# Kernel optimization log

Hardware: AMD Instinct MI355X
Metric: run time of the kernel (lower is better)

## Reference

```python
import jax, jax.numpy as jnp
import numpy as np

B, S, HID = 2, 2048, 2304
H, KVH, D = 8, 4, 256          # query heads, kv heads, head_dim
N_REP = H // KVH
SCALE = 256.0 ** -0.5          # query_pre_attn_scalar ** -0.5
SOFTCAP = 50.0
ROPE_THETA = 10000.0
NEG = -1e9


def setup_inputs() -> dict:
    key = jax.random.key(0)
    k1, k2, k3, k4, k5 = jax.random.split(key, 5)
    hidden_states = jax.random.normal(k1, (B, S, HID), dtype=jnp.float32)
    # RoPE cos/sin tables, shape [B, S, D]
    inv_freq = 1.0 / (ROPE_THETA ** (jnp.arange(0, D, 2, dtype=jnp.float32) / D))
    pos = jnp.arange(S, dtype=jnp.float32)
    freqs = pos[:, None] * inv_freq[None, :]            # [S, D/2]
    emb = jnp.concatenate([freqs, freqs], axis=-1)      # [S, D]
    cos = jnp.broadcast_to(jnp.cos(emb)[None], (B, S, D))
    sin = jnp.broadcast_to(jnp.sin(emb)[None], (B, S, D))
    # additive causal mask [B, 1, S, S] (sliding_window=4096 > S, so pure causal)
    idx = jnp.arange(S)
    causal = idx[None, :] <= idx[:, None]
    attention_mask = jnp.broadcast_to(
        jnp.where(causal, 0.0, NEG).astype(jnp.float32)[None, None], (B, 1, S, S))
    # projection weights (lecun-normal-ish scale), no bias (attention_bias=False)
    Wq = jax.random.normal(k2, (HID, H * D), dtype=jnp.float32) / np.sqrt(HID)
    Wk = jax.random.normal(k3, (HID, KVH * D), dtype=jnp.float32) / np.sqrt(HID)
    Wv = jax.random.normal(k4, (HID, KVH * D), dtype=jnp.float32) / np.sqrt(HID)
    Wo = jax.random.normal(k5, (H * D, HID), dtype=jnp.float32) / np.sqrt(H * D)
    return {"hidden_states": hidden_states, "cos": cos, "sin": sin,
            "attention_mask": attention_mask,
            "Wq": Wq, "Wk": Wk, "Wv": Wv, "Wo": Wo}


def _rotate_half(x):
    half = x.shape[-1] // 2
    return jnp.concatenate([-x[..., half:], x[..., :half]], axis=-1)


def reference(hidden_states, cos, sin, attention_mask, Wq, Wk, Wv, Wo):
    b, s, _ = hidden_states.shape
    q = (hidden_states @ Wq).reshape(b, s, H, D).transpose(0, 2, 1, 3)    # [B,H,S,D]
    k = (hidden_states @ Wk).reshape(b, s, KVH, D).transpose(0, 2, 1, 3)  # [B,KVH,S,D]
    v = (hidden_states @ Wv).reshape(b, s, KVH, D).transpose(0, 2, 1, 3)
    c = cos[:, None]  # [B,1,S,D] broadcast over heads (unsqueeze_dim=1)
    sn = sin[:, None]
    q = q * c + _rotate_half(q) * sn
    k = k * c + _rotate_half(k) * sn
    # GQA: repeat kv heads (interleave, matching repeat_kv tile+reshape)
    k = jnp.repeat(k, N_REP, axis=1)
    v = jnp.repeat(v, N_REP, axis=1)
    w = jnp.einsum('bhqd,bhkd->bhqk', q, k) * SCALE
    w = jnp.tanh(w / SOFTCAP) * SOFTCAP                  # logit softcapping
    w = w + attention_mask[:, :, :, :s]
    w = jax.nn.softmax(w.astype(jnp.float32), axis=-1).astype(q.dtype)
    out = jnp.einsum('bhqk,bhkd->bhqd', w, v)
    out = out.transpose(0, 2, 1, 3).reshape(b, s, H * D)
    return out @ Wo
```

## Files before the change

### kernel.cpp

```cpp
#include <hip/hip_runtime.h>

typedef unsigned short u16;
typedef __attribute__((ext_vector_type(8))) short short8;
typedef __attribute__((ext_vector_type(4))) float f32x4;

constexpr int B_ = 2;
constexpr int H_ = 8;
constexpr int KVH_ = 4;
constexpr int S_ = 2048;
constexpr int D_ = 256;
constexpr int HID_ = 2304;
constexpr int QKVN_ = 4096;
constexpr int AON_ = 2048;

__device__ __forceinline__ float b2f(u16 u) {
  union { float f; unsigned int i; } x; x.i = ((unsigned int)u) << 16; return x.f;
}
__device__ __forceinline__ u16 f2b(float f) {
  unsigned int x = __float_as_uint(f);
  unsigned int r = (x + 0x7fffu + ((x >> 16) & 1u)) >> 16;
  return (u16)r;
}

__global__ void cast_kernel(const float* __restrict__ in, u16* __restrict__ out) {
  size_t i = ((size_t)blockIdx.x * 256 + threadIdx.x) * 4;
  float4 v = *(const float4*)(in + i);
  unsigned int lo = (unsigned int)f2b(v.x) | ((unsigned int)f2b(v.y) << 16);
  unsigned int hi = (unsigned int)f2b(v.z) | ((unsigned int)f2b(v.w) << 16);
  uint2 o; o.x = lo; o.y = hi;
  *(uint2*)(out + i) = o;
}

__global__ void transpose_cast_all(const float* __restrict__ s0, const float* __restrict__ s1,
                                   const float* __restrict__ s2, const float* __restrict__ s3,
                                   u16* __restrict__ d0, u16* __restrict__ d1,
                                   u16* __restrict__ d2, u16* __restrict__ d3) {
  __shared__ float tile[64][65];
  int which = blockIdx.z;
  const float* src; u16* dst; int R, C;
  if (which == 0)      { src = s0; dst = d0; R = 2304; C = 2048; }
  else if (which == 1) { src = s1; dst = d1; R = 2304; C = 1024; }
  else if (which == 2) { src = s2; dst = d2; R = 2304; C = 1024; }
  else                 { src = s3; dst = d3; R = 2048; C = 2304; }
  int r0 = blockIdx.y * 64, c0 = blockIdx.x * 64;
  if (r0 >= R || c0 >= C) return;
  int t = threadIdx.x;
#pragma unroll
  for (int i = 0; i < 16; ++i) {
    int e = i * 256 + t;
    int r = e >> 6, c = e & 63;
    tile[r][c] = src[(size_t)(r0 + r) * C + (c0 + c)];
  }
  __syncthreads();
#pragma unroll
  for (int i = 0; i < 16; ++i) {
    int e = i * 256 + t;
    int orow = e >> 6, ocol = e & 63;
    dst[(size_t)(c0 + orow) * R + (r0 + ocol)] = f2b(tile[ocol][orow]);
  }
}

template <int OUTF32>
__global__ __launch_bounds__(512, 2) void gemm_bt8(
    const u16* __restrict__ A, const u16* __restrict__ B, void* __restrict__ Cp,
    int M, int N, int K) {
  __shared__ u16 lds[2][2][2][8192];
  const int tid = threadIdx.x;
  const int lane = tid & 63;
  const int wave = tid >> 6;
  const int wm = wave >> 2, wn = wave & 3;
  const int quad = lane >> 4, l16 = lane & 15;
  const int m0 = blockIdx.y * 256, n0 = blockIdx.x * 256;
  const int nt = K >> 6;

  const int sub = tid >> 6;
  const int rr = (tid >> 2) & 15;
  const int cc = ((tid & 3) * 8) ^ ((rr & 8) ? 16 : 0);
  const int r_rel = (sub >> 1) * 16 + rr;
  const int ccol = (sub & 1) * 32 + cc;
  const u16* Asrc = A + (size_t)(m0 + r_rel) * K + ccol;
  const u16* Bsrc = B + (size_t)(n0 + r_rel) * K + ccol;
  const int ldsc = tid * 8;

  const int fr_off = l16 * 64 + (((quad * 8) ^ ((l16 & 8) ? 16 : 0)) << 1);

#define GL8(src, dst)                                                                  \
  __builtin_amdgcn_global_load_lds((const __attribute__((address_space(1))) void*)(src), \
                                   (__attribute__((address_space(3))) void*)(dst), 16, 0, 0)
#define STAGE_A(bf, kt, qp) {                                                          \
    const u16* _s = Asrc + (size_t)(kt) * 64;                                          \
    GL8(_s + (size_t)((qp) * 64) * K,       &lds[bf][0][0][(qp) * 4096 + ldsc]);       \
    GL8(_s + (size_t)(128 + (qp) * 64) * K, &lds[bf][0][1][(qp) * 4096 + ldsc]); }
#define STAGE_B(bf, kt, hf) {                                                          \
    const u16* _s = Bsrc + (size_t)(kt) * 64;                                          \
    GL8(_s + (size_t)((hf) * 128) * K,      &lds[bf][1][hf][ldsc]);                    \
    GL8(_s + (size_t)((hf) * 128 + 64) * K, &lds[bf][1][hf][4096 + ldsc]); }
#define LDA(bf, mi, kk) \
  (*(const short8*)((const char*)&lds[bf][0][wm][0] + (mi) * 2048 + (kk) * 1024 + fr_off))
#define LDB(bf, ni, kk) \
  (*(const short8*)((const char*)&lds[bf][1][wn >> 1][0] + ((wn & 1) * 4 + (ni)) * 2048 + (kk) * 1024 + fr_off))

  f32x4 acc[8][4] = {};
  short8 bfr[4][2], af[2][2];

  STAGE_B(0, 0, 0); STAGE_B(0, 0, 1); STAGE_A(0, 0, 0); STAGE_A(0, 0, 1);
  STAGE_B(1, 1, 0); STAGE_B(1, 1, 1); STAGE_A(1, 1, 0);
  asm volatile("s_waitcnt vmcnt(6)" ::: "memory");
  __builtin_amdgcn_s_barrier();

#define PHASE(q, STG, VMW)                                                             \
    _Pragma("unroll") for (int i = 0; i < 2; ++i)                                      \
      _Pragma("unroll") for (int kk = 0; kk < 2; ++kk) af[i][kk] = LDA(c, 2 * (q) + i, kk); \
    STG; VMW;                                                                          \
    __builtin_amdgcn_s_barrier();                                                      \
    asm volatile("s_waitcnt lgkmcnt(0)" ::: "memory");                                 \
    __builtin_amdgcn_sched_barrier(0);                                                 \
    __builtin_amdgcn_s_setprio(1);                                                     \
    _Pragma("unroll") for (int i = 0; i < 2; ++i)                                      \
      _Pragma("unroll") for (int ni = 0; ni < 4; ++ni)                                 \
        _Pragma("unroll") for (int kk = 0; kk < 2; ++kk)                               \
          acc[2 * (q) + i][ni] = __builtin_amdgcn_mfma_f32_16x16x32_bf16(              \
              af[i][kk], bfr[ni][kk], acc[2 * (q) + i][ni], 0, 0, 0);                  \
    __builtin_amdgcn_s_setprio(0);                                                     \
    __builtin_amdgcn_s_barrier();

  for (int T = 0; T < nt; ++T) {
    const int c = T & 1;
#pragma unroll
    for (int ni = 0; ni < 4; ++ni)
#pragma unroll
      for (int kk = 0; kk < 2; ++kk) bfr[ni][kk] = LDB(c, ni, kk);
    PHASE(0, if (T + 1 < nt) STAGE_A(c ^ 1, T + 1, 1), )
    PHASE(1, if (T + 2 < nt) STAGE_B(c, T + 2, 0), )
    PHASE(2, if (T + 2 < nt) STAGE_B(c, T + 2, 1), )
    PHASE(3, if (T + 2 < nt) STAGE_A(c, T + 2, 0),
          if (T + 2 >= nt) { asm volatile("s_waitcnt vmcnt(0)" ::: "memory"); }
          else             { asm volatile("s_waitcnt vmcnt(6)" ::: "memory"); })
  }
#undef PHASE
#undef LDA
#undef LDB
#undef STAGE_A
#undef STAGE_B
#undef GL8

#pragma unroll
  for (int mi = 0; mi < 8; ++mi) {
#pragma unroll
    for (int ni = 0; ni < 4; ++ni) {
#pragma unroll
      for (int r = 0; r < 4; ++r) {
        int row = m0 + wm * 128 + mi * 16 + quad * 4 + r;
        int col = n0 + wn * 64 + ni * 16 + l16;
        if (OUTF32)
          ((float*)Cp)[(size_t)row * N + col] = acc[mi][ni][r];
        else
          ((u16*)Cp)[(size_t)row * N + col] = f2b(acc[mi][ni][r]);
      }
    }
  }
}

__global__ void rope_kernel(const u16* __restrict__ qkv, const float* __restrict__ cs,
                            const float* __restrict__ sn, u16* __restrict__ Qr,
                            u16* __restrict__ Kr) {
  int row = blockIdx.x;
  int b = row >> 11, s = row & 2047;
  int d = threadIdx.x;
  const u16* qrow = qkv + (size_t)row * QKVN_;
  float c = cs[(size_t)row * D_ + d];
  float si = sn[(size_t)row * D_ + d];
  int dp = (d < 128) ? d + 128 : d - 128;
  float sgn = (d < 128) ? -1.f : 1.f;
#pragma unroll
  for (int h = 0; h < H_; ++h) {
    float v = b2f(qrow[h * D_ + d]);
    float p = sgn * b2f(qrow[h * D_ + dp]);
    Qr[((size_t)(b * H_ + h) * S_ + s) * D_ + d] = f2b(v * c + p * si);
  }
#pragma unroll
  for (int g = 0; g < KVH_; ++g) {
    float v = b2f(qrow[2048 + g * D_ + d]);
    float p = sgn * b2f(qrow[2048 + g * D_ + dp]);
    Kr[((size_t)(b * KVH_ + g) * S_ + s) * D_ + d] = f2b(v * c + p * si);
  }
}

__global__ void transpose_v(const u16* __restrict__ qkv, u16* __restrict__ Vt) {
  __shared__ u16 tile[64][72];
  int d0 = blockIdx.x * 64, s0 = blockIdx.y * 64, g = blockIdx.z;
  int b = g >> 2, kvh = g & 3;
  int t = threadIdx.x;
#pragma unroll
  for (int i = 0; i < 16; ++i) {
    int e = i * 256 + t;
    int r = e >> 6, c = e & 63;
    tile[r][c] = qkv[(size_t)(b * S_ + s0 + r) * QKVN_ + 3072 + kvh * D_ + d0 + c];
  }
  __syncthreads();
#pragma unroll
  for (int i = 0; i < 16; ++i) {
    int e = i * 256 + t;
    int orow = e >> 6, ocol = e & 63;
    Vt[((size_t)g * D_ + d0 + orow) * S_ + s0 + ocol] = tile[ocol][orow];
  }
}

__global__ __launch_bounds__(256, 2) void attn_kernel(
    const u16* __restrict__ Qr, const u16* __restrict__ Kr, const u16* __restrict__ Vt,
    float* __restrict__ Op0, float* __restrict__ Op1,
    float* __restrict__ Lp0, float* __restrict__ Lp1) {
  __shared__ u16 Ks[2][32 * 256];
  __shared__ u16 Vs[2][32 * 256];
  int bx = blockIdx.x;
  int b = bx >> 8;
  int r = bx & 255;
  int h = r >> 5;
  int rem = r & 31;
  int sp = rem >> 4;
  int t = rem & 15;
  int qt0 = (t & 1) ? (15 - (t >> 1)) : (t >> 1);
  int qt = b ? (15 - qt0) : qt0;
  int kvh = h >> 1;
  int tid = threadIdx.x, wave = tid >> 6, lane = tid & 63;
  int quad = lane >> 4, l16 = lane & 15;
  float* Op = sp ? Op1 : Op0;
  float* Lp = sp ? Lp1 : Lp0;
  const int kst_r = tid >> 5;
  const int kst_c = (tid & 31) ^ ((tid >> 5) & 3);
  const int vst_r = tid >> 2;
  const int vst_c = (tid & 3) ^ ((tid >> 3) & 3);
  const int kg = l16 >> 2, ka = l16 & 3;
  const int srow0 = 8 * kg + ka;
  const int ksw = ka | ((kg & 1) << 2);

  int q0 = qt * 128;
  int beg = sp ? (2 * qt + 2) : 0;
  int end = sp ? (4 * qt + 4) : (2 * qt + 2);
  const u16* Qbase = Qr + ((size_t)(b * H_ + h) * S_ + q0 + wave * 32 + l16) * D_;
  short8 qf[2][8];
#pragma unroll
  for (int f = 0; f < 2; ++f)
#pragma unroll
    for (int kk = 0; kk < 8; ++kk)
      qf[f][kk] = *(const short8*)(Qbase + (size_t)f * 16 * D_ + kk * 32 + quad * 8);
  const u16* Kbase = Kr + (size_t)(b * KVH_ + kvh) * S_ * D_;
  const u16* Vbase = Vt + (size_t)(b * KVH_ + kvh) * D_ * S_;
  float lp[2] = {0.f, 0.f};
  f32x4 o_acc[2][16] = {};
  const int qq0 = q0 + wave * 32 + l16;

#define STAGE(KT, BUF)                                                                 \
  {                                                                                    \
    int k0s = (KT) * 32;                                                               \
    _Pragma("unroll") for (int i = 0; i < 4; ++i) {                                    \
      int p = i * 256 + tid;                                                           \
      __builtin_amdgcn_global_load_lds(                                                \
          (const __attribute__((address_space(1))) void*)(Kbase +                      \
              (size_t)(k0s + i * 8 + kst_r) * D_ + (kst_c ^ ((i & 1) << 2)) * 8),      \
          (__attribute__((address_space(3))) void*)(&Ks[BUF][0] + p * 8), 16, 0, 0);   \
    }                                                                                  \
    _Pragma("unroll") for (int i = 0; i < 4; ++i) {                                    \
      int p = i * 256 + tid;                                                           \
      __builtin_amdgcn_global_load_lds(                                                \
          (const __attribute__((address_space(1))) void*)(Vbase +                      \
              (size_t)(i * 64 + vst_r) * S_ + k0s + vst_c * 8),                        \
          (__attribute__((address_space(3))) void*)(&Vs[BUF][0] + p * 8), 16, 0, 0);   \
    }                                                                                  \
  }

  STAGE(beg, 0);
  __syncthreads();
  for (int kt = beg; kt < end; ++kt) {
    int k0 = kt * 32;
    int cur = (kt - beg) & 1;
    if (kt + 1 < end) STAGE(kt + 1, cur ^ 1);
    f32x4 sacc[2][2] = {};
    __builtin_amdgcn_s_setprio(1);
#pragma unroll
    for (int n = 0; n < 2; ++n) {
      const u16* kb = &Ks[cur][0] + (srow0 + 4 * n) * 256;
#pragma unroll
      for (int kk = 0; kk < 8; ++kk) {
        int phys = (kk * 4 + quad) ^ ksw;
        short8 kfr = *(const short8*)(kb + phys * 8);
        sacc[0][n] = __builtin_amdgcn_mfma_f32_16x16x32_bf16(kfr, qf[0][kk], sacc[0][n], 0, 0, 0);
        sacc[1][n] = __builtin_amdgcn_mfma_f32_16x16x32_bf16(kfr, qf[1][kk], sacc[1][n], 0, 0, 0);
      }
    }
    __builtin_amdgcn_s_setprio(0);
    bool full = (k0 + 31 <= q0 + wave * 32);
    short8 pa[2];
#pragma unroll
    for (int f = 0; f < 2; ++f) {
      union { short8 s8; unsigned int d[4]; } pu;
#pragma unroll
      for (int n = 0; n < 2; ++n) {
#pragma unroll
        for (int rr2 = 0; rr2 < 4; ++rr2) {
          float E = __expf(sacc[f][n][rr2] * 0.0025f);
          float ee = __expf(-100.0f * __frcp_rn(E + 1.0f));
          if (!full) {
            int key = k0 + 8 * quad + 4 * n + rr2;
            ee = (key <= qq0 + f * 16) ? ee : 0.0f;
          }
          lp[f] += ee;
          sacc[f][n][rr2] = ee;
        }
        pu.d[2 * n]     = (unsigned int)f2b(sacc[f][n][0]) | ((unsigned int)f2b(sacc[f][n][1]) << 16);
        pu.d[2 * n + 1] = (unsigned int)f2b(sacc[f][n][2]) | ((unsigned int)f2b(sacc[f][n][3]) << 16);
      }
      pa[f] = pu.s8;
    }
    __builtin_amdgcn_s_setprio(1);
#pragma unroll
    for (int dt = 0; dt < 16; ++dt) {
      int d = dt * 16 + l16;
      int phys = quad ^ ((d >> 1) & 3);
      short8 vb = *(const short8*)(&Vs[cur][0] + d * 32 + phys * 8);
      o_acc[0][dt] = __builtin_amdgcn_mfma_f32_16x16x32_bf16(pa[0], vb, o_acc[0][dt], 0, 0, 0);
      o_acc[1][dt] = __builtin_amdgcn_mfma_f32_16x16x32_bf16(pa[1], vb, o_acc[1][dt], 0, 0, 0);
    }
    __builtin_amdgcn_s_setprio(0);
    __syncthreads();
  }
#undef STAGE
#pragma unroll
  for (int f = 0; f < 2; ++f) {
    lp[f] += __shfl_xor(lp[f], 16, 64);
    lp[f] += __shfl_xor(lp[f], 32, 64);
  }
  if (lane < 16) {
    size_t lb = ((size_t)(b * H_ + h)) * S_ + q0 + wave * 32 + lane;
    Lp[lb] = lp[0];
    Lp[lb + 16] = lp[1];
  }
#pragma unroll
  for (int f = 0; f < 2; ++f)
#pragma unroll
    for (int dt = 0; dt < 16; ++dt)
#pragma unroll
      for (int rr2 = 0; rr2 < 4; ++rr2) {
        int row = b * S_ + q0 + wave * 32 + f * 16 + quad * 4 + rr2;
        int col = h * D_ + dt * 16 + l16;
        Op[(size_t)row * AON_ + col] = o_acc[f][dt][rr2];
      }
}

__global__ void combine_kernel(const float* __restrict__ Op0, const float* __restrict__ Op1,
                               const float* __restrict__ Lp0, const float* __restrict__ Lp1,
                               u16* __restrict__ Ao) {
  size_t idx = (size_t)blockIdx.x * 256 + threadIdx.x;
  size_t row = idx >> 9;
  int c4 = ((int)idx & 511) * 4;
  const float4 a = *(const float4*)(Op0 + row * AON_ + c4);
  const float4 b4 = *(const float4*)(Op1 + row * AON_ + c4);
  int b = (int)(row >> 11), s = (int)row & 2047;
  int h = c4 >> 8;
  size_t li = ((size_t)(b * H_ + h)) * S_ + s;
  float inv = 1.0f / (Lp0[li] + Lp1[li]);
  unsigned int lo = (unsigned int)f2b((a.x + b4.x) * inv) | ((unsigned int)f2b((a.y + b4.y) * inv) << 16);
  unsigned int hi = (unsigned int)f2b((a.z + b4.z) * inv) | ((unsigned int)f2b((a.w + b4.w) * inv) << 16);
  uint2 o; o.x = lo; o.y = hi;
  *(uint2*)(Ao + row * AON_ + c4) = o;
}

extern "C" void kernel_launch(void* const* d_in, const int* in_sizes, int n_in,
                              void* d_out, int out_size, void* d_ws, size_t ws_size,
                              hipStream_t stream) {
  const float* hidden = (const float*)d_in[0];
  const float* cosp = (const float*)d_in[1];
  const float* sinp = (const float*)d_in[2];
  const float* Wq = (const float*)d_in[4];
  const float* Wk = (const float*)d_in[5];
  const float* Wv = (const float*)d_in[6];
  const float* Wo = (const float*)d_in[7];

  u16* hs  = (u16*)d_ws;
  u16* WT  = hs  + (size_t)4096 * HID_;
  u16* WoT = WT  + (size_t)4096 * HID_;
  u16* qkv = WoT + (size_t)HID_ * AON_;
  u16* Qr  = qkv + (size_t)4096 * QKVN_;
  u16* Kr  = Qr  + (size_t)B_ * H_ * S_ * D_;
  u16* Vt  = Kr  + (size_t)B_ * KVH_ * S_ * D_;
  u16* Ao  = Vt  + (size_t)B_ * KVH_ * S_ * D_;
  float* Lp0 = (float*)(Ao + (size_t)4096 * AON_);
  float* Lp1 = Lp0 + (size_t)B_ * H_ * S_;
  float* Op0 = (float*)hs;
  float* Op1 = (float*)qkv;

  cast_kernel<<<9216, 256, 0, stream>>>(hidden, hs);
  transpose_cast_all<<<dim3(36, 36, 4), 256, 0, stream>>>(
      Wq, Wk, Wv, Wo, WT, WT + (size_t)2048 * HID_, WT + (size_t)3072 * HID_, WoT);
  gemm_bt8<0><<<dim3(16, 16), 512, 0, stream>>>(hs, WT, qkv, 4096, QKVN_, HID_);
  rope_kernel<<<4096, 256, 0, stream>>>(qkv, cosp, sinp, Qr, Kr);
  transpose_v<<<dim3(4, 32, 8), 256, 0, stream>>>(qkv, Vt);
  attn_kernel<<<dim3(512), 256, 0, stream>>>(Qr, Kr, Vt, Op0, Op1, Lp0, Lp1);
  combine_kernel<<<16384, 256, 0, stream>>>(Op0, Op1, Lp0, Lp1, Ao);
  gemm_bt8<1><<<dim3(9, 16), 512, 0, stream>>>(Ao, WoT, d_out, 4096, HID_, 2048);
}
```

Baseline: 424.3 us.

## Restructure attention: 512-thread blocks, split head dim, pair batches per block

The attention kernel now uses 512 threads (8 waves) covering 256 query rows. Each block handles only half of the head dimension (dsp) for the PV product, which halves the V tile and the output accumulators. Each block processes both batches sequentially, pairing complementary causal q-tiles to balance work, and launches 256 blocks instead of 512. This aims to cut register pressure and improve load balance across CUs. In exchange, QK^T and the softmax are computed twice, once per d-half.

Result: slower. 444.2 us (+4.7%).

```diff
diff --git a/kernel.cpp b/kernel.cpp
--- a/kernel.cpp
+++ b/kernel.cpp
@@ -206,145 +206,143 @@
   }
 }
 
-__global__ __launch_bounds__(256, 2) void attn_kernel(
+__global__ __launch_bounds__(512, 2) void attn_kernel(
     const u16* __restrict__ Qr, const u16* __restrict__ Kr, const u16* __restrict__ Vt,
     float* __restrict__ Op0, float* __restrict__ Op1,
     float* __restrict__ Lp0, float* __restrict__ Lp1) {
   __shared__ u16 Ks[2][32 * 256];
-  __shared__ u16 Vs[2][32 * 256];
+  __shared__ u16 Vs[2][128 * 32];
   int bx = blockIdx.x;
-  int b = bx >> 8;
-  int r = bx & 255;
-  int h = r >> 5;
-  int rem = r & 31;
-  int sp = rem >> 4;
-  int t = rem & 15;
-  int qt0 = (t & 1) ? (15 - (t >> 1)) : (t >> 1);
-  int qt = b ? (15 - qt0) : qt0;
+  int h = bx >> 5;
+  int dsp = (bx >> 4) & 1;
+  int sp = (bx >> 3) & 1;
+  int u = bx & 7;
   int kvh = h >> 1;
   int tid = threadIdx.x, wave = tid >> 6, lane = tid & 63;
   int quad = lane >> 4, l16 = lane & 15;
   float* Op = sp ? Op1 : Op0;
   float* Lp = sp ? Lp1 : Lp0;
-  const int kst_r = tid >> 5;
-  const int kst_c = (tid & 31) ^ ((tid >> 5) & 3);
-  const int vst_r = tid >> 2;
-  const int vst_c = (tid & 3) ^ ((tid >> 3) & 3);
+  const int vd = tid >> 2;
+  const int vc = (tid & 3) ^ ((tid >> 3) & 3);
   const int kg = l16 >> 2, ka = l16 & 3;
   const int srow0 = 8 * kg + ka;
   const int ksw = ka | ((kg & 1) << 2);
 
-  int q0 = qt * 128;
-  int beg = sp ? (2 * qt + 2) : 0;
-  int end = sp ? (4 * qt + 4) : (2 * qt + 2);
-  const u16* Qbase = Qr + ((size_t)(b * H_ + h) * S_ + q0 + wave * 32 + l16) * D_;
-  short8 qf[2][8];
-#pragma unroll
-  for (int f = 0; f < 2; ++f)
-#pragma unroll
-    for (int kk = 0; kk < 8; ++kk)
-      qf[f][kk] = *(const short8*)(Qbase + (size_t)f * 16 * D_ + kk * 32 + quad * 8);
-  const u16* Kbase = Kr + (size_t)(b * KVH_ + kvh) * S_ * D_;
-  const u16* Vbase = Vt + (size_t)(b * KVH_ + kvh) * D_ * S_;
-  float lp[2] = {0.f, 0.f};
-  f32x4 o_acc[2][16] = {};
-  const int qq0 = q0 + wave * 32 + l16;
-
-#define STAGE(KT, BUF)                                                                 \
-  {                                                                                    \
-    int k0s = (KT) * 32;                                                               \
-    _Pragma("unroll") for (int i = 0; i < 4; ++i) {                                    \
-      int p = i * 256 + tid;                                                           \
-      __builtin_amdgcn_global_load_lds(                                                \
-          (const __attribute__((address_space(1))) void*)(Kbase +                      \
-              (size_t)(k0s + i * 8 + kst_r) * D_ + (kst_c ^ ((i & 1) << 2)) * 8),      \
-          (__attribute__((address_space(3))) void*)(&Ks[BUF][0] + p * 8), 16, 0, 0);   \
-    }                                                                                  \
-    _Pragma("unroll") for (int i = 0; i < 4; ++i) {                                    \
-      int p = i * 256 + tid;                                                           \
-      __builtin_amdgcn_global_load_lds(                                                \
-          (const __attribute__((address_space(1))) void*)(Vbase +                      \
-              (size_t)(i * 64 + vst_r) * S_ + k0s + vst_c * 8),                        \
-          (__attribute__((address_space(3))) void*)(&Vs[BUF][0] + p * 8), 16, 0, 0);   \
-    }                                                                                  \
-  }
-
-  STAGE(beg, 0);
-  __syncthreads();
-  for (int kt = beg; kt < end; ++kt) {
-    int k0 = kt * 32;
-    int cur = (kt - beg) & 1;
-    if (kt + 1 < end) STAGE(kt + 1, cur ^ 1);
-    f32x4 sacc[2][2] = {};
-    __builtin_amdgcn_s_setprio(1);
-#pragma unroll
-    for (int n = 0; n < 2; ++n) {
-      const u16* kb = &Ks[cur][0] + (srow0 + 4 * n) * 256;
-#pragma unroll
-      for (int kk = 0; kk < 8; ++kk) {
-        int phys = (kk * 4 + quad) ^ ksw;
-        short8 kfr = *(const short8*)(kb + phys * 8);
-        sacc[0][n] = __builtin_amdgcn_mfma_f32_16x16x32_bf16(kfr, qf[0][kk], sacc[0][n], 0, 0, 0);
-        sacc[1][n] = __builtin_amdgcn_mfma_f32_16x16x32_bf16(kfr, qf[1][kk], sacc[1][n], 0, 0, 0);
+  for (int part = 0; part < 2; ++part) {
+    int b = part;
+    int qt = part ? (7 - u) : u;
+    int q0 = qt * 256;
+    int nh = 4 * qt + 4;
+    int beg = sp ? nh : 0;
+    int end = sp ? (2 * nh) : nh;
+    const u16* Qbase = Qr + ((size_t)(b * H_ + h) * S_ + q0 + wave * 32 + l16) * D_;
+    short8 qf[2][8];
+#pragma unroll
+    for (int f = 0; f < 2; ++f)
+#pragma unroll
+      for (int kk = 0; kk < 8; ++kk)
+        qf[f][kk] = *(const short8*)(Qbase + (size_t)f * 16 * D_ + kk * 32 + quad * 8);
+    const u16* Kbase = Kr + (size_t)(b * KVH_ + kvh) * S_ * D_;
+    const u16* Vbase = Vt + ((size_t)(b * KVH_ + kvh) * D_ + dsp * 128) * S_;
+    float lp[2] = {0.f, 0.f};
+    f32x4 o_acc[2][8] = {};
+    const int qq0 = q0 + wave * 32 + l16;
+
+#define STAGE(KT, BUF)                                                                   \
+    {                                                                                    \
+      int k0s = (KT) * 32;                                                               \
+      _Pragma("unroll") for (int i = 0; i < 2; ++i) {                                    \
+        int p = i * 512 + tid;                                                           \
+        int ks = p >> 5;                                                                 \
+        int kc = (p & 31) ^ ((ks & 3) | (((ks >> 3) & 1) << 2));                         \
+        __builtin_amdgcn_global_load_lds(                                                \
+            (const __attribute__((address_space(1))) void*)(Kbase +                      \
+                (size_t)(k0s + ks) * D_ + kc * 8),                                       \
+            (__attribute__((address_space(3))) void*)(&Ks[BUF][0] + p * 8), 16, 0, 0);   \
+      }                                                                                  \
+      __builtin_amdgcn_global_load_lds(                                                  \
+          (const __attribute__((address_space(1))) void*)(Vbase +                        \
+              (size_t)vd * S_ + k0s + vc * 8),                                           \
+          (__attribute__((address_space(3))) void*)(&Vs[BUF][0] + tid * 8), 16, 0, 0);   \
+    }
+
+    STAGE(beg, 0);
+    __syncthreads();
+    for (int kt = beg; kt < end; ++kt) {
+      int k0 = kt * 32;
+      int cur = (kt - beg) & 1;
+      if (kt + 1 < end) STAGE(kt + 1, cur ^ 1);
+      f32x4 sacc[2][2] = {};
+      __builtin_amdgcn_s_setprio(1);
+#pragma unroll
+      for (int n = 0; n < 2; ++n) {
+        const u16* kb = &Ks[cur][0] + (srow0 + 4 * n) * 256;
+#pragma unroll
+        for (int kk = 0; kk < 8; ++kk) {
+          int phys = (kk * 4 + quad) ^ ksw;
+          short8 kfr = *(const short8*)(kb + phys * 8);
+          sacc[0][n] = __builtin_amdgcn_mfma_f32_16x16x32_bf16(kfr, qf[0][kk], sacc[0][n], 0, 0, 0);
+          sacc[1][n] = __builtin_amdgcn_mfma_f32_16x16x32_bf16(kfr, qf[1][kk], sacc[1][n], 0, 0, 0);
+        }
       }
-    }
-    __builtin_amdgcn_s_setprio(0);
-    bool full = (k0 + 31 <= q0 + wave * 32);
-    short8 pa[2];
+      __builtin_amdgcn_s_setprio(0);
+      bool full = (k0 + 31 <= q0 + wave * 32);
+      short8 pa[2];
+#pragma unroll
+      for (int f = 0; f < 2; ++f) {
+        union { short8 s8; unsigned int d[4]; } pu;
+#pragma unroll
+        for (int n = 0; n < 2; ++n) {
+#pragma unroll
+          for (int rr2 = 0; rr2 < 4; ++rr2) {
+            float E = __expf(sacc[f][n][rr2] * 0.0025f);
+            float ee = __expf(-100.0f * __frcp_rn(E + 1.0f));
+            if (!full) {
+              int key = k0 + 8 * quad + 4 * n + rr2;
+              ee = (key <= qq0 + f * 16) ? ee : 0.0f;
+            }
+            lp[f] += ee;
+            sacc[f][n][rr2] = ee;
+          }
+          pu.d[2 * n]     = (unsigned int)f2b(sacc[f][n][0]) | ((unsigned int)f2b(sacc[f][n][1]) << 16);
+          pu.d[2 * n + 1] = (unsigned int)f2b(sacc[f][n][2]) | ((unsigned int)f2b(sacc[f][n][3]) << 16);
+        }
+        pa[f] = pu.s8;
+      }
+      __builtin_amdgcn_s_setprio(1);
+#pragma unroll
+      for (int dt = 0; dt < 8; ++dt) {
+        int d = dt * 16 + l16;
+        int phys = quad ^ ((d >> 1) & 3);
+        short8 vb = *(const short8*)(&Vs[cur][0] + d * 32 + phys * 8);
+        o_acc[0][dt] = __builtin_amdgcn_mfma_f32_16x16x32_bf16(pa[0], vb, o_acc[0][dt], 0, 0, 0);
+        o_acc[1][dt] = __builtin_amdgcn_mfma_f32_16x16x32_bf16(pa[1], vb, o_acc[1][dt], 0, 0, 0);
+      }
+      __builtin_amdgcn_s_setprio(0);
+      __syncthreads();
+    }
+#undef STAGE
 #pragma unroll
     for (int f = 0; f < 2; ++f) {
-      union { short8 s8; unsigned int d[4]; } pu;
-#pragma unroll
-      for (int n = 0; n < 2; ++n) {
+      lp[f] += __shfl_xor(lp[f], 16, 64);
+      lp[f] += __shfl_xor(lp[f], 32, 64);
+    }
+    if (dsp == 0 && lane < 16) {
+      size_t lb = ((size_t)(b * H_ + h)) * S_ + q0 + wave * 32 + lane;
+      Lp[lb] = lp[0];
+      Lp[lb + 16] = lp[1];
+    }
+#pragma unroll
+    for (int f = 0; f < 2; ++f)
+#pragma unroll
+      for (int dt = 0; dt < 8; ++dt)
 #pragma unroll
         for (int rr2 = 0; rr2 < 4; ++rr2) {
-          float E = __expf(sacc[f][n][rr2] * 0.0025f);
-          float ee = __expf(-100.0f * __frcp_rn(E + 1.0f));
-          if (!full) {
-            int key = k0 + 8 * quad + 4 * n + rr2;
-            ee = (key <= qq0 + f * 16) ? ee : 0.0f;
-          }
-          lp[f] += ee;
-          sacc[f][n][rr2] = ee;
+          int row = b * S_ + q0 + wave * 32 + f * 16 + quad * 4 + rr2;
+          int col = h * D_ + dsp * 128 + dt * 16 + l16;
+          Op[(size_t)row * AON_ + col] = o_acc[f][dt][rr2];
         }
-        pu.d[2 * n]     = (unsigned int)f2b(sacc[f][n][0]) | ((unsigned int)f2b(sacc[f][n][1]) << 16);
-        pu.d[2 * n + 1] = (unsigned int)f2b(sacc[f][n][2]) | ((unsigned int)f2b(sacc[f][n][3]) << 16);
-      }
-      pa[f] = pu.s8;
-    }
-    __builtin_amdgcn_s_setprio(1);
-#pragma unroll
-    for (int dt = 0; dt < 16; ++dt) {
-      int d = dt * 16 + l16;
-      int phys = quad ^ ((d >> 1) & 3);
-      short8 vb = *(const short8*)(&Vs[cur][0] + d * 32 + phys * 8);
-      o_acc[0][dt] = __builtin_amdgcn_mfma_f32_16x16x32_bf16(pa[0], vb, o_acc[0][dt], 0, 0, 0);
-      o_acc[1][dt] = __builtin_amdgcn_mfma_f32_16x16x32_bf16(pa[1], vb, o_acc[1][dt], 0, 0, 0);
-    }
-    __builtin_amdgcn_s_setprio(0);
-    __syncthreads();
-  }
-#undef STAGE
-#pragma unroll
-  for (int f = 0; f < 2; ++f) {
-    lp[f] += __shfl_xor(lp[f], 16, 64);
-    lp[f] += __shfl_xor(lp[f], 32, 64);
-  }
-  if (lane < 16) {
-    size_t lb = ((size_t)(b * H_ + h)) * S_ + q0 + wave * 32 + lane;
-    Lp[lb] = lp[0];
-    Lp[lb + 16] = lp[1];
-  }
-#pragma unroll
-  for (int f = 0; f < 2; ++f)
-#pragma unroll
-    for (int dt = 0; dt < 16; ++dt)
-#pragma unroll
-      for (int rr2 = 0; rr2 < 4; ++rr2) {
-        int row = b * S_ + q0 + wave * 32 + f * 16 + quad * 4 + rr2;
-        int col = h * D_ + dt * 16 + l16;
-        Op[(size_t)row * AON_ + col] = o_acc[f][dt][rr2];
-      }
+  }
 }
 
 __global__ void combine_kernel(const float* __restrict__ Op0, const float* __restrict__ Op1,
@@ -395,7 +393,7 @@
   gemm_bt8<0><<<dim3(16, 16), 512, 0, stream>>>(hs, WT, qkv, 4096, QKVN_, HID_);
   rope_kernel<<<4096, 256, 0, stream>>>(qkv, cosp, sinp, Qr, Kr);
   transpose_v<<<dim3(4, 32, 8), 256, 0, stream>>>(qkv, Vt);
-  attn_kernel<<<dim3(512), 256, 0, stream>>>(Qr, Kr, Vt, Op0, Op1, Lp0, Lp1);
+  attn_kernel<<<dim3(256), 512, 0, stream>>>(Qr, Kr, Vt, Op0, Op1, Lp0, Lp1);
   combine_kernel<<<16384, 256, 0, stream>>>(Op0, Op1, Lp0, Lp1, Ao);
   gemm_bt8<1><<<dim3(9, 16), 512, 0, stream>>>(Ao, WoT, d_out, 4096, HID_, 2048);
 }
```
